# Kernel optimization log

Measured on AMD Instinct MI355X. Metric: run time of the kernel, lower is better.

Reference implementation:

```python
import jax, jax.numpy as jnp
import numpy as np

DIM = 768
NUM_HEADS = 12
HEAD_DIM = DIM // NUM_HEADS
B, N = 16, 784


def setup_inputs() -> dict:
    key = jax.random.key(0)
    k1, k2, k3, k4, k5 = jax.random.split(key, 5)
    x = jax.random.normal(k1, (B, N, DIM), dtype=jnp.float32)
    # Dense params (flax Dense: kernel [in, out], bias [out])
    Wqkv = jax.random.normal(k2, (DIM, 3 * DIM), dtype=jnp.float32) * (DIM ** -0.5)
    bqkv = jnp.zeros((3 * DIM,), dtype=jnp.float32)
    Wo = jax.random.normal(k3, (DIM, DIM), dtype=jnp.float32) * (DIM ** -0.5)
    bo = jnp.zeros((DIM,), dtype=jnp.float32)
    return {"x": x, "Wqkv": Wqkv, "bqkv": bqkv, "Wo": Wo, "bo": bo}


def reference(x, Wqkv, bqkv, Wo, bo):
    b, n, dim = x.shape
    # fused QKV projection
    qkv = jnp.einsum('bnd,df->bnf', x, Wqkv) + bqkv          # [b, n, 3*dim]
    qkv = qkv.reshape(b, n, 3, NUM_HEADS, HEAD_DIM)           # '(k h d)' split
    q, k, v = qkv[:, :, 0], qkv[:, :, 1], qkv[:, :, 2]        # [b, n, h, d]
    scale = HEAD_DIM ** -0.5
    # chunked/flash path computes exact softmax attention; same math, expressed densely
    scores = jnp.einsum('bihd,bjhd->bhij', q, k) * scale      # [b, h, n, n]
    attn = jax.nn.softmax(scores, axis=-1)
    out = jnp.einsum('bhij,bjhd->bihd', attn, v)              # [b, n, h, d]
    out = out.reshape(b, n, dim)                              # 'b n (h d)'
    return jnp.einsum('bnd,df->bnf', out, Wo) + bo
```

## Files before the change

### kernel.cpp

```cpp
#include <hip/hip_runtime.h>

#define DIM 768
#define NHEADS 12
#define HDIM 64
#define BB 16
#define NN 784
#define M_TOTAL (BB * NN)

typedef __attribute__((ext_vector_type(8))) _Float16 f16x8;
typedef __attribute__((ext_vector_type(4))) float f32x4;

typedef __attribute__((address_space(3))) unsigned int lds_uint;
typedef __attribute__((address_space(1))) const unsigned int g_uint;
__device__ inline void gload_lds16(const void* g, void* l) {
    __builtin_amdgcn_global_load_lds((g_uint*)(uintptr_t)g,
                                     (lds_uint*)(uintptr_t)l, 16, 0, 0);
}

__global__ __launch_bounds__(256) void cvt_f16_kernel(
    const float* __restrict__ in, _Float16* __restrict__ out, int n)
{
    int i = (blockIdx.x * 256 + threadIdx.x) * 8;
    if (i >= n) return;
    float4 a = *(const float4*)&in[i];
    float4 b = *(const float4*)&in[i + 4];
    union { _Float16 h[8]; uint4 v; } o;
    o.h[0] = (_Float16)a.x; o.h[1] = (_Float16)a.y;
    o.h[2] = (_Float16)a.z; o.h[3] = (_Float16)a.w;
    o.h[4] = (_Float16)b.x; o.h[5] = (_Float16)b.y;
    o.h[6] = (_Float16)b.z; o.h[7] = (_Float16)b.w;
    *(uint4*)&out[i] = o.v;
}

__global__ __launch_bounds__(256) void transpose_f16_kernel(
    const float* __restrict__ W, _Float16* __restrict__ T, int K, int N)
{
    __shared__ float t[32][33];
    const int n0 = blockIdx.x * 32, k0 = blockIdx.y * 32;
    const int r = threadIdx.x >> 3, c4 = (threadIdx.x & 7) * 4;
    float4 v = *(const float4*)&W[(size_t)(k0 + r) * N + n0 + c4];
    t[r][c4 + 0] = v.x; t[r][c4 + 1] = v.y;
    t[r][c4 + 2] = v.z; t[r][c4 + 3] = v.w;
    __syncthreads();
    union { _Float16 h[4]; ushort4 v4; } o;
#pragma unroll
    for (int i = 0; i < 4; ++i) o.h[i] = (_Float16)t[c4 + i][r];
    *(ushort4*)&T[(size_t)(n0 + r) * K + k0 + c4] = o.v4;
}

template <int OUT_F16>
__global__ __launch_bounds__(256) void gemm_f16_kernel(
    const _Float16* __restrict__ A, const _Float16* __restrict__ B,
    const float* __restrict__ bias, void* __restrict__ Cout,
    int M, int N, int K)
{
    __shared__ _Float16 sA[128 * 32];
    __shared__ _Float16 sB[128 * 32];

    const int tid  = threadIdx.x;
    const int wave = tid >> 6;
    const int lane = tid & 63;
    const int gm = blockIdx.y * 128;
    const int gn = blockIdx.x * 128;
    const int wm = (wave & 1) * 64;
    const int wn = (wave >> 1) * 64;
    const int quad = lane >> 4;
    const int l16  = lane & 15;

    const int r0 = wave * 32 + (lane >> 2);
    const int c0 = (lane & 3) * 8;

    f32x4 acc[4][4] = {};

    for (int k0 = 0; k0 < K; k0 += 32) {
        __syncthreads();
        gload_lds16(A + (size_t)(gm + r0) * K + k0 + c0,      &sA[r0 * 32 + c0]);
        gload_lds16(A + (size_t)(gm + r0 + 16) * K + k0 + c0, &sA[(r0 + 16) * 32 + c0]);
        gload_lds16(B + (size_t)(gn + r0) * K + k0 + c0,      &sB[r0 * 32 + c0]);
        gload_lds16(B + (size_t)(gn + r0 + 16) * K + k0 + c0, &sB[(r0 + 16) * 32 + c0]);
        __syncthreads();

        f16x8 a[4];
#pragma unroll
        for (int mt = 0; mt < 4; ++mt)
            a[mt] = *(const f16x8*)&sA[(wm + mt * 16 + l16) * 32 + quad * 8];
#pragma unroll
        for (int nt = 0; nt < 4; ++nt) {
            f16x8 b = *(const f16x8*)&sB[(wn + nt * 16 + l16) * 32 + quad * 8];
#pragma unroll
            for (int mt = 0; mt < 4; ++mt)
                acc[mt][nt] = __builtin_amdgcn_mfma_f32_16x16x32_f16(a[mt], b, acc[mt][nt], 0, 0, 0);
        }
    }

#pragma unroll
    for (int nt = 0; nt < 4; ++nt) {
        const int col = gn + wn + nt * 16 + l16;
        const float bv = bias[col];
#pragma unroll
        for (int mt = 0; mt < 4; ++mt) {
            f32x4 v = acc[mt][nt];
#pragma unroll
            for (int r = 0; r < 4; ++r) {
                const int row = gm + wm + mt * 16 + quad * 4 + r;
                const float o = v[r] + bv;
                if (OUT_F16)
                    ((_Float16*)Cout)[(size_t)row * N + col] = (_Float16)o;
                else
                    ((float*)Cout)[(size_t)row * N + col] = o;
            }
        }
    }
}

#define LOG2E_8 0.18033688f

#define ATTN_TILE(J0, TAIL)                                                    \
  {                                                                            \
    const int j0_ = (J0);                                                      \
    int jrowK = j0_ + sj;                                                      \
    if (TAIL && jrowK > NN - 1) jrowK = NN - 1;                                \
    const size_t kbase = (size_t)(b * NN + jrowK) * (3 * DIM) + DIM + h * HDIM;\
    uint4 k0v = *(const uint4*)&qkv[kbase + sg * 8];                           \
    uint4 k1v = *(const uint4*)&qkv[kbase + sg * 8 + 32];                      \
    int vr0 = j0_ + 2 * jj, vr1 = j0_ + 2 * jj + 1;                            \
    if (TAIL) { if (vr0 > NN - 1) vr0 = NN - 1; if (vr1 > NN - 1) vr1 = NN - 1; } \
    const size_t vb0 = (size_t)(b * NN + vr0) * (3 * DIM) + 2 * DIM + h * HDIM + dsub; \
    const size_t vb1 = (size_t)(b * NN + vr1) * (3 * DIM) + 2 * DIM + h * HDIM + dsub; \
    union { uint4 v; _Float16 h[8]; } va, vc;                                  \
    va.v = *(const uint4*)&qkv[vb0];                                           \
    vc.v = *(const uint4*)&qkv[vb1];                                           \
    __syncthreads();                                                           \
    *(uint4*)&Ks[sj][sg * 8]      = k0v;                                       \
    *(uint4*)&Ks[sj][sg * 8 + 32] = k1v;                                       \
    _Pragma("unroll")                                                          \
    for (int i = 0; i < 8; ++i) {                                              \
        union { _Float16 h[2]; unsigned int u; } t;                            \
        t.h[0] = va.h[i]; t.h[1] = vc.h[i];                                    \
        *(unsigned int*)&Vt[dsub + i][2 * jj] = t.u;                           \
    }                                                                          \
    __syncthreads();                                                           \
    f32x4 s[4] = {};                                                           \
    _Pragma("unroll")                                                          \
    for (int nt = 0; nt < 4; ++nt) {                                           \
        f16x8 kf0 = *(const f16x8*)&Ks[nt * 16 + l16][quad * 8];               \
        f16x8 kf1 = *(const f16x8*)&Ks[nt * 16 + l16][32 + quad * 8];          \
        s[nt] = __builtin_amdgcn_mfma_f32_16x16x32_f16(qfrag[0], kf0, s[nt], 0, 0, 0); \
        s[nt] = __builtin_amdgcn_mfma_f32_16x16x32_f16(qfrag[1], kf1, s[nt], 0, 0, 0); \
    }                                                                          \
    _Pragma("unroll")                                                          \
    for (int nt = 0; nt < 4; ++nt)                                             \
        _Pragma("unroll")                                                      \
        for (int r = 0; r < 4; ++r) {                                          \
            float pv = exp2f(s[nt][r]);                                        \
            if (TAIL && (j0_ + nt * 16) >= NN) pv = 0.f;                       \
            lpart[r] += pv;                                                    \
            Ph[wave * 16 + quad * 4 + r][nt * 16 + l16] = (_Float16)pv;        \
        }                                                                      \
    _Pragma("unroll")                                                          \
    for (int ks = 0; ks < 2; ++ks) {                                           \
        f16x8 ph = *(const f16x8*)&Ph[wave * 16 + l16][ks * 32 + quad * 8];    \
        _Pragma("unroll")                                                      \
        for (int dt = 0; dt < 4; ++dt) {                                       \
            f16x8 vf = *(const f16x8*)&Vt[dt * 16 + l16][ks * 32 + quad * 8];  \
            O[dt] = __builtin_amdgcn_mfma_f32_16x16x32_f16(ph, vf, O[dt], 0, 0, 0); \
        }                                                                      \
    }                                                                          \
  }

__global__ __launch_bounds__(256) void attn_f16_kernel(
    const _Float16* __restrict__ qkv, _Float16* __restrict__ oat)
{
    const int b = blockIdx.z;
    const int h = blockIdx.y;
    const int q0 = blockIdx.x * 64;
    const int tid = threadIdx.x;
    const int wave = tid >> 6;
    const int lane = tid & 63;
    const int quad = lane >> 4;
    const int l16  = lane & 15;

    __shared__ _Float16 Ks[64][72];
    __shared__ _Float16 Vt[64][72];
    __shared__ _Float16 Ph[64][72];

    f16x8 qfrag[2];
    {
        int qrow = q0 + wave * 16 + l16; if (qrow > NN - 1) qrow = NN - 1;
        size_t base = (size_t)(b * NN + qrow) * (3 * DIM) + h * HDIM;
        f16x8 q0v = *(const f16x8*)&qkv[base + quad * 8];
        f16x8 q1v = *(const f16x8*)&qkv[base + 32 + quad * 8];
        qfrag[0] = q0v * (_Float16)LOG2E_8;
        qfrag[1] = q1v * (_Float16)LOG2E_8;
    }

    const int sj = lane;
    const int sg = wave;
    const int jj   = lane & 31;
    const int dsub = sg * 16 + (lane >> 5) * 8;

    f32x4 O[4] = {};
    float lpart[4] = {};

    for (int jt = 0; jt < 12; ++jt) {
        ATTN_TILE(jt * 64, 0)
    }
    ATTN_TILE(768, 1)

    float lrow[4];
#pragma unroll
    for (int r = 0; r < 4; ++r) {
        float t = lpart[r];
        t += __shfl_xor(t, 1);
        t += __shfl_xor(t, 2);
        t += __shfl_xor(t, 4);
        t += __shfl_xor(t, 8);
        lrow[r] = t;
    }

#pragma unroll
    for (int r = 0; r < 4; ++r) {
        const int q = q0 + wave * 16 + quad * 4 + r;
        if (q < NN) {
            const float inv = 1.0f / lrow[r];
#pragma unroll
            for (int dt = 0; dt < 4; ++dt) {
                const size_t base = (size_t)(b * NN + q) * DIM + h * HDIM + dt * 16 + l16;
                oat[base] = (_Float16)(O[dt][r] * inv);
            }
        }
    }
}

extern "C" void kernel_launch(void* const* d_in, const int* in_sizes, int n_in,
                              void* d_out, int out_size, void* d_ws, size_t ws_size,
                              hipStream_t stream) {
    const float* x    = (const float*)d_in[0];
    const float* Wqkv = (const float*)d_in[1];
    const float* bqkv = (const float*)d_in[2];
    const float* Wo   = (const float*)d_in[3];
    const float* bo   = (const float*)d_in[4];
    float* out = (float*)d_out;

    _Float16* qkv = (_Float16*)d_ws;
    _Float16* xh  = qkv + (size_t)M_TOTAL * 3 * DIM;
    _Float16* wqT = xh + (size_t)M_TOTAL * DIM;
    _Float16* woT = wqT + (size_t)3 * DIM * DIM;
    _Float16* oat = xh;

    {
        int n = M_TOTAL * DIM;
        cvt_f16_kernel<<<n / 8 / 256, 256, 0, stream>>>(x, xh, n);
    }
    transpose_f16_kernel<<<dim3((3 * DIM) / 32, DIM / 32), 256, 0, stream>>>(
        Wqkv, wqT, DIM, 3 * DIM);
    transpose_f16_kernel<<<dim3(DIM / 32, DIM / 32), 256, 0, stream>>>(
        Wo, woT, DIM, DIM);
    gemm_f16_kernel<1><<<dim3((3 * DIM) / 128, M_TOTAL / 128), 256, 0, stream>>>(
        xh, wqT, bqkv, qkv, M_TOTAL, 3 * DIM, DIM);
    attn_f16_kernel<<<dim3(13, NHEADS, BB), 256, 0, stream>>>(qkv, oat);
    gemm_f16_kernel<0><<<dim3(DIM / 128, M_TOTAL / 128), 256, 0, stream>>>(
        oat, woT, bo, out, M_TOTAL, DIM, DIM);
}
```

Measured before the change: 279.5 us.

## Use 32x32x16 MFMA with K=64 tiles and XOR-swizzled LDS in GEMM

The projection GEMM now stages 64-wide K slices per iteration instead of 32, which halves the number of barrier pairs. It switches from 16x16x32 to 32x32x16 MFMA tiles, giving each wave a 2x2 block of 32x32 tiles. LDS columns are XOR-swizzled on write and read to avoid bank conflicts. The aim is fewer LDS reads per MFMA and less synchronization, at the cost of twice the LDS footprint and a changed epilogue store pattern.

Result: faster. 272.0 us (-2.7%).

```diff
diff --git a/kernel.cpp b/kernel.cpp
--- a/kernel.cpp
+++ b/kernel.cpp
@@ -9,6 +9,7 @@
 
 typedef __attribute__((ext_vector_type(8))) _Float16 f16x8;
 typedef __attribute__((ext_vector_type(4))) float f32x4;
+typedef __attribute__((ext_vector_type(16))) float f32x16;
 
 typedef __attribute__((address_space(3))) unsigned int lds_uint;
 typedef __attribute__((address_space(1))) const unsigned int g_uint;
@@ -54,8 +55,8 @@
     const float* __restrict__ bias, void* __restrict__ Cout,
     int M, int N, int K)
 {
-    __shared__ _Float16 sA[128 * 32];
-    __shared__ _Float16 sB[128 * 32];
+    __shared__ _Float16 sA[128 * 64];
+    __shared__ _Float16 sB[128 * 64];
 
     const int tid  = threadIdx.x;
     const int wave = tid >> 6;
@@ -64,46 +65,57 @@
     const int gn = blockIdx.x * 128;
     const int wm = (wave & 1) * 64;
     const int wn = (wave >> 1) * 64;
-    const int quad = lane >> 4;
-    const int l16  = lane & 15;
-
-    const int r0 = wave * 32 + (lane >> 2);
-    const int c0 = (lane & 3) * 8;
-
-    f32x4 acc[4][4] = {};
-
-    for (int k0 = 0; k0 < K; k0 += 32) {
+    const int l31 = lane & 31;
+    const int hi  = lane >> 5;
+
+    const int srow = lane >> 3;
+    const int scol = (((lane & 7) ^ (srow & 7)) * 8);
+
+    f32x16 acc[2][2] = {};
+
+    for (int k0 = 0; k0 < K; k0 += 64) {
         __syncthreads();
-        gload_lds16(A + (size_t)(gm + r0) * K + k0 + c0,      &sA[r0 * 32 + c0]);
-        gload_lds16(A + (size_t)(gm + r0 + 16) * K + k0 + c0, &sA[(r0 + 16) * 32 + c0]);
-        gload_lds16(B + (size_t)(gn + r0) * K + k0 + c0,      &sB[r0 * 32 + c0]);
-        gload_lds16(B + (size_t)(gn + r0 + 16) * K + k0 + c0, &sB[(r0 + 16) * 32 + c0]);
+#pragma unroll
+        for (int i = 0; i < 4; ++i) {
+            const int rbase = wave * 32 + i * 8;
+            gload_lds16(A + (size_t)(gm + rbase + srow) * K + k0 + scol,
+                        &sA[rbase * 64]);
+            gload_lds16(B + (size_t)(gn + rbase + srow) * K + k0 + scol,
+                        &sB[rbase * 64]);
+        }
         __syncthreads();
 
-        f16x8 a[4];
-#pragma unroll
-        for (int mt = 0; mt < 4; ++mt)
-            a[mt] = *(const f16x8*)&sA[(wm + mt * 16 + l16) * 32 + quad * 8];
-#pragma unroll
-        for (int nt = 0; nt < 4; ++nt) {
-            f16x8 b = *(const f16x8*)&sB[(wn + nt * 16 + l16) * 32 + quad * 8];
-#pragma unroll
-            for (int mt = 0; mt < 4; ++mt)
-                acc[mt][nt] = __builtin_amdgcn_mfma_f32_16x16x32_f16(a[mt], b, acc[mt][nt], 0, 0, 0);
-        }
-    }
-
-#pragma unroll
-    for (int nt = 0; nt < 4; ++nt) {
-        const int col = gn + wn + nt * 16 + l16;
+#pragma unroll
+        for (int kk = 0; kk < 4; ++kk) {
+            const int c = kk * 2 + hi;
+            const int sw = (c ^ (l31 & 7)) * 8;
+            f16x8 a[2], bf[2];
+#pragma unroll
+            for (int mt = 0; mt < 2; ++mt)
+                a[mt] = *(const f16x8*)&sA[(wm + mt * 32 + l31) * 64 + sw];
+#pragma unroll
+            for (int nt = 0; nt < 2; ++nt)
+                bf[nt] = *(const f16x8*)&sB[(wn + nt * 32 + l31) * 64 + sw];
+#pragma unroll
+            for (int mt = 0; mt < 2; ++mt)
+#pragma unroll
+                for (int nt = 0; nt < 2; ++nt)
+                    acc[mt][nt] = __builtin_amdgcn_mfma_f32_32x32x16_f16(
+                        a[mt], bf[nt], acc[mt][nt], 0, 0, 0);
+        }
+    }
+
+#pragma unroll
+    for (int nt = 0; nt < 2; ++nt) {
+        const int col = gn + wn + nt * 32 + l31;
         const float bv = bias[col];
 #pragma unroll
-        for (int mt = 0; mt < 4; ++mt) {
-            f32x4 v = acc[mt][nt];
-#pragma unroll
-            for (int r = 0; r < 4; ++r) {
-                const int row = gm + wm + mt * 16 + quad * 4 + r;
-                const float o = v[r] + bv;
+        for (int mt = 0; mt < 2; ++mt) {
+            f32x16 v = acc[mt][nt];
+#pragma unroll
+            for (int reg = 0; reg < 16; ++reg) {
+                const int row = gm + wm + mt * 32 + (reg & 3) + 8 * (reg >> 2) + 4 * hi;
+                const float o = v[reg] + bv;
                 if (OUT_F16)
                     ((_Float16*)Cout)[(size_t)row * N + col] = (_Float16)o;
                 else
```
